# Performance work log

Measured on AMD Instinct MI355X. Metric: run time of the kernel, lower is better.

## Reference

```python
import jax, jax.numpy as jnp
import numpy as np

MAX_H = 512
MAX_W = 512
N_INST = 100
MASK_HW = 28


def _bilinear_sample(img, gx, gy):
    """grid_sample, mode='bilinear', padding_mode='zeros', align_corners=False.
    img: [B, H, W] float; gx, gy: [B, Ho, Wo] normalized coords in [-1, 1].
    Returns [B, Ho, Wo].
    """
    H, W = img.shape[1], img.shape[2]
    # unnormalize (align_corners=False)
    x = (gx + 1.0) * (W * 0.5) - 0.5
    y = (gy + 1.0) * (H * 0.5) - 0.5
    x0f = jnp.floor(x)
    y0f = jnp.floor(y)
    x0 = x0f.astype(jnp.int32)
    y0 = y0f.astype(jnp.int32)
    x1 = x0 + 1
    y1 = y0 + 1
    wx1 = x - x0f
    wx0 = 1.0 - wx1
    wy1 = y - y0f
    wy0 = 1.0 - wy1

    def gather(yi, xi):
        valid = (yi >= 0) & (yi < H) & (xi >= 0) & (xi < W)
        yc = jnp.clip(yi, 0, H - 1)
        xc = jnp.clip(xi, 0, W - 1)
        v = jax.vmap(lambda im, yy, xx: im[yy, xx])(img, yc, xc)
        return jnp.where(valid, v, jnp.zeros((), img.dtype))

    v00 = gather(y0, x0)
    v01 = gather(y0, x1)
    v10 = gather(y1, x0)
    v11 = gather(y1, x1)
    return (v00 * (wy0 * wx0) + v01 * (wy0 * wx1)
            + v10 * (wy1 * wx0) + v11 * (wy1 * wx1))


def setup_inputs() -> dict:
    key = jax.random.key(0)
    k1, k2, k3 = jax.random.split(key, 3)
    masks = jax.random.uniform(k1, (N_INST, 1, MASK_HW, MASK_HW), dtype=jnp.float32)
    # valid boxes inside the 512x512 canvas: x1 > x0, y1 > y0
    cxy = jax.random.uniform(k2, (N_INST, 2), minval=80.0, maxval=432.0)
    wh = jax.random.uniform(k3, (N_INST, 2), minval=32.0, maxval=256.0)
    x0y0 = jnp.clip(cxy - wh * 0.5, 0.0, MAX_W - 1.0)
    x1y1 = jnp.clip(cxy + wh * 0.5, 1.0, MAX_W - 1.0)
    boxes = jnp.concatenate([x0y0, x1y1], axis=1).astype(jnp.float32)
    return {"masks": masks, "boxes": boxes}


def reference(masks, boxes) -> jnp.ndarray:
    N, C, H, W = masks.shape
    m = masks.reshape(N * C, H, W).astype(jnp.float32)
    b = boxes.reshape(-1, 4)
    x0 = b[:, 0:1]
    y0 = b[:, 1:2]
    x1 = b[:, 2:3] + 1e-5
    y1 = b[:, 3:4] + 1e-5
    img_y = jnp.arange(MAX_H, dtype=jnp.float32) + 0.5  # [MAX_H]
    img_x = jnp.arange(MAX_W, dtype=jnp.float32) + 0.5  # [MAX_W]
    gy1d = (img_y[None, :] - y0) / (y1 - y0) * 2.0 - 1.0  # [B, MAX_H]
    gx1d = (img_x[None, :] - x0) / (x1 - x0) * 2.0 - 1.0  # [B, MAX_W]
    B = N * C
    gx = jnp.broadcast_to(gx1d[:, None, :], (B, MAX_H, MAX_W))
    gy = jnp.broadcast_to(gy1d[:, :, None], (B, MAX_H, MAX_W))
    out = _bilinear_sample(m, gx, gy)  # [B, MAX_H, MAX_W]
    return out.reshape(N, C, MAX_H, MAX_W)
```

## Files before the change

### kernel.cpp

```cpp
#include <hip/hip_runtime.h>

#define MASK_HW 28
#define OUT_H 512
#define OUT_W 512
#define ROWS_PER_BLOCK 16

__global__ __launch_bounds__(256) void paste_masks_kernel(
    const float* __restrict__ masks,
    const float* __restrict__ boxes,
    float* __restrict__ out)
{
    __shared__ float sm[31][33];
    const int n   = blockIdx.y;
    const int tid = threadIdx.x;

    for (int i = tid; i < 31 * 33; i += 256) ((float*)sm)[i] = 0.0f;
    __syncthreads();
    const float* mptr = masks + (size_t)n * (MASK_HW * MASK_HW);
    for (int i = tid; i < MASK_HW * MASK_HW; i += 256) {
        int r = i / MASK_HW;
        int c = i - r * MASK_HW;
        sm[r + 1][c + 1] = mptr[i];
    }

    const float bx0 = boxes[4 * n + 0];
    const float by0 = boxes[4 * n + 1];
    const float bx1 = boxes[4 * n + 2] + 1e-5f;
    const float by1 = boxes[4 * n + 3] + 1e-5f;
    const float sxf = 28.0f / (bx1 - bx0);
    const float syf = 28.0f / (by1 - by0);
    __syncthreads();

    const int row0 = blockIdx.x * ROWS_PER_BLOCK;
    float* outn = out + (size_t)n * (OUT_H * OUT_W);

    const int chunks = ROWS_PER_BLOCK * (OUT_W / 4);
    for (int cid = tid; cid < chunks; cid += 256) {
        const int r   = cid >> 7;
        const int xq  = cid & 127;
        const int row = row0 + r;

        const float ys = ((float)row + 0.5f - by0) * syf - 0.5f;
        float4 v = make_float4(0.f, 0.f, 0.f, 0.f);

        if (ys > -1.0f && ys < 28.0f) {
            const float y0f = floorf(ys);
            const int   y0i = (int)y0f;
            const float wy1 = ys - y0f;
            const float wy0 = 1.0f - wy1;
            const float* r0 = &sm[y0i + 1][0];
            const float* r1 = &sm[y0i + 2][0];

            const float xbase = (float)(xq * 4) + 0.5f - bx0;
            float res[4];
            #pragma unroll
            for (int j = 0; j < 4; ++j) {
                const float xs = (xbase + (float)j) * sxf - 0.5f;
                float val = 0.0f;
                if (xs > -1.0f && xs < 28.0f) {
                    const float x0f = floorf(xs);
                    const int   x0i = (int)x0f;
                    const float wx1 = xs - x0f;
                    const float wx0 = 1.0f - wx1;
                    const float v00 = r0[x0i + 1];
                    const float v01 = r0[x0i + 2];
                    const float v10 = r1[x0i + 1];
                    const float v11 = r1[x0i + 2];
                    val = wy0 * (wx0 * v00 + wx1 * v01) +
                          wy1 * (wx0 * v10 + wx1 * v11);
                }
                res[j] = val;
            }
            v = make_float4(res[0], res[1], res[2], res[3]);
        }
        *reinterpret_cast<float4*>(outn + (size_t)row * OUT_W + xq * 4) = v;
    }
}

extern "C" void kernel_launch(void* const* d_in, const int* in_sizes, int n_in,
                              void* d_out, int out_size, void* d_ws, size_t ws_size,
                              hipStream_t stream) {
    const float* masks = (const float*)d_in[0];
    const float* boxes = (const float*)d_in[1];
    float* out = (float*)d_out;

    dim3 grid(OUT_H / ROWS_PER_BLOCK, 100);
    dim3 block(256);
    paste_masks_kernel<<<grid, block, 0, stream>>>(masks, boxes, out);
}
```

Measured before the change: 112.5 us.

## Split into bulk zero-fill kernel and box-restricted bilinear paste kernel

The single kernel that interpolated every output pixel is replaced by two launches. A grid-stride kernel writes zeros over the whole output with float4 stores, then a second kernel computes bilinear values only inside each box's clipped row and column range. Row tiles that fall outside the box exit early, and shared-memory loading moves after that bounds check. The cost is a second launch, pixels inside each box being written twice, and scalar rather than float4 stores in the paste kernel.

Measured after the change: 121.9 us. +8.3%, slower.

```diff
diff --git a/kernel.cpp b/kernel.cpp
--- a/kernel.cpp
+++ b/kernel.cpp
@@ -3,25 +3,24 @@
 #define MASK_HW 28
 #define OUT_H 512
 #define OUT_W 512
-#define ROWS_PER_BLOCK 16
+#define N_INST 100
+#define ROWS_PER_TILE 16
 
-__global__ __launch_bounds__(256) void paste_masks_kernel(
+__global__ __launch_bounds__(256) void zero_fill_kernel(float4* __restrict__ out, int n4)
+{
+    const int stride = gridDim.x * 256;
+    const float4 z = make_float4(0.f, 0.f, 0.f, 0.f);
+    for (int i = blockIdx.x * 256 + threadIdx.x; i < n4; i += stride)
+        out[i] = z;
+}
+
+__global__ __launch_bounds__(256) void paste_box_kernel(
     const float* __restrict__ masks,
     const float* __restrict__ boxes,
     float* __restrict__ out)
 {
-    __shared__ float sm[31][33];
-    const int n   = blockIdx.y;
+    const int n   = blockIdx.x;
     const int tid = threadIdx.x;
-
-    for (int i = tid; i < 31 * 33; i += 256) ((float*)sm)[i] = 0.0f;
-    __syncthreads();
-    const float* mptr = masks + (size_t)n * (MASK_HW * MASK_HW);
-    for (int i = tid; i < MASK_HW * MASK_HW; i += 256) {
-        int r = i / MASK_HW;
-        int c = i - r * MASK_HW;
-        sm[r + 1][c + 1] = mptr[i];
-    }
 
     const float bx0 = boxes[4 * n + 0];
     const float by0 = boxes[4 * n + 1];
@@ -29,51 +28,60 @@
     const float by1 = boxes[4 * n + 3] + 1e-5f;
     const float sxf = 28.0f / (bx1 - bx0);
     const float syf = 28.0f / (by1 - by0);
+    const float inv_sx = (bx1 - bx0) * (1.0f / 28.0f);
+    const float inv_sy = (by1 - by0) * (1.0f / 28.0f);
+
+    const float xlo = bx0 - 0.5f - 0.5f * inv_sx;
+    const float xhi = bx0 - 0.5f + 28.5f * inv_sx;
+    const float ylo = by0 - 0.5f - 0.5f * inv_sy;
+    const float yhi = by0 - 0.5f + 28.5f * inv_sy;
+
+    const int clo = max(0, (int)floorf(xlo));
+    const int chi = min(OUT_W, (int)ceilf(xhi) + 1);
+    const int rlo = max(0, (int)floorf(ylo));
+    const int rhi = min(OUT_H, (int)ceilf(yhi) + 1);
+
+    const int r0 = rlo + blockIdx.y * ROWS_PER_TILE;
+    if (r0 >= rhi) return;
+    const int r1 = min(r0 + ROWS_PER_TILE, rhi);
+
+    __shared__ float sm[MASK_HW + 2][MASK_HW + 5];
+    for (int i = tid; i < (MASK_HW + 2) * (MASK_HW + 5); i += 256)
+        ((float*)sm)[i] = 0.0f;
+    __syncthreads();
+    const float* mptr = masks + (size_t)n * (MASK_HW * MASK_HW);
+    for (int i = tid; i < MASK_HW * MASK_HW; i += 256) {
+        const int r = i / MASK_HW;
+        const int c = i - r * MASK_HW;
+        sm[r + 1][c + 1] = mptr[i];
+    }
     __syncthreads();
 
-    const int row0 = blockIdx.x * ROWS_PER_BLOCK;
     float* outn = out + (size_t)n * (OUT_H * OUT_W);
 
-    const int chunks = ROWS_PER_BLOCK * (OUT_W / 4);
-    for (int cid = tid; cid < chunks; cid += 256) {
-        const int r   = cid >> 7;
-        const int xq  = cid & 127;
-        const int row = row0 + r;
+    for (int row = r0; row < r1; ++row) {
+        const float ys = ((float)row + 0.5f - by0) * syf - 0.5f;
+        if (ys <= -1.0f || ys >= 28.0f) continue;
+        const float y0f = floorf(ys);
+        const int   y0i = (int)y0f;
+        const float wy1 = ys - y0f;
+        const float wy0 = 1.0f - wy1;
+        const float* rA = &sm[y0i + 1][0];
+        const float* rB = &sm[y0i + 2][0];
 
-        const float ys = ((float)row + 0.5f - by0) * syf - 0.5f;
-        float4 v = make_float4(0.f, 0.f, 0.f, 0.f);
-
-        if (ys > -1.0f && ys < 28.0f) {
-            const float y0f = floorf(ys);
-            const int   y0i = (int)y0f;
-            const float wy1 = ys - y0f;
-            const float wy0 = 1.0f - wy1;
-            const float* r0 = &sm[y0i + 1][0];
-            const float* r1 = &sm[y0i + 2][0];
-
-            const float xbase = (float)(xq * 4) + 0.5f - bx0;
-            float res[4];
-            #pragma unroll
-            for (int j = 0; j < 4; ++j) {
-                const float xs = (xbase + (float)j) * sxf - 0.5f;
-                float val = 0.0f;
-                if (xs > -1.0f && xs < 28.0f) {
-                    const float x0f = floorf(xs);
-                    const int   x0i = (int)x0f;
-                    const float wx1 = xs - x0f;
-                    const float wx0 = 1.0f - wx1;
-                    const float v00 = r0[x0i + 1];
-                    const float v01 = r0[x0i + 2];
-                    const float v10 = r1[x0i + 1];
-                    const float v11 = r1[x0i + 2];
-                    val = wy0 * (wx0 * v00 + wx1 * v01) +
-                          wy1 * (wx0 * v10 + wx1 * v11);
-                }
-                res[j] = val;
+        for (int c = clo + tid; c < chi; c += 256) {
+            const float xs = ((float)c + 0.5f - bx0) * sxf - 0.5f;
+            float val = 0.0f;
+            if (xs > -1.0f && xs < 28.0f) {
+                const float x0f = floorf(xs);
+                const int   x0i = (int)x0f;
+                const float wx1 = xs - x0f;
+                const float wx0 = 1.0f - wx1;
+                val = wy0 * (wx0 * rA[x0i + 1] + wx1 * rA[x0i + 2]) +
+                      wy1 * (wx0 * rB[x0i + 1] + wx1 * rB[x0i + 2]);
             }
-            v = make_float4(res[0], res[1], res[2], res[3]);
+            outn[(size_t)row * OUT_W + c] = val;
         }
-        *reinterpret_cast<float4*>(outn + (size_t)row * OUT_W + xq * 4) = v;
     }
 }
 
@@ -84,7 +92,8 @@
     const float* boxes = (const float*)d_in[1];
     float* out = (float*)d_out;
 
-    dim3 grid(OUT_H / ROWS_PER_BLOCK, 100);
-    dim3 block(256);
-    paste_masks_kernel<<<grid, block, 0, stream>>>(masks, boxes, out);
+    const int n4 = N_INST * OUT_H * OUT_W / 4;
+    zero_fill_kernel<<<dim3(2048), dim3(256), 0, stream>>>((float4*)out, n4);
+
+    paste_box_kernel<<<dim3(N_INST, 17), dim3(256), 0, stream>>>(masks, boxes, out);
 }
```

## Drop shared-memory staging and gather mask texels directly from global

Applied to the files above, without the earlier changes.

Removes the per-block shared-memory tile, its zero-fill and both barriers. Each thread now reads the four mask texels straight from global memory (served by cache), using clamped indices with zeroed weights for border handling. The grid becomes one float4 per thread with a flat 1D launch, and threads whose row falls outside the box store zeros and exit early. The cost is more global and cache loads per output in exchange for less block setup and synchronisation in a store-bound kernel.

Measured after the change: 117.9 us. +4.8%, slower.

```diff
diff --git a/kernel.cpp b/kernel.cpp
--- a/kernel.cpp
+++ b/kernel.cpp
@@ -3,78 +3,70 @@
 #define MASK_HW 28
 #define OUT_H 512
 #define OUT_W 512
-#define ROWS_PER_BLOCK 16
+#define N_INST 100
 
-__global__ __launch_bounds__(256) void paste_masks_kernel(
+typedef __attribute__((ext_vector_type(4))) float f32x4;
+
+__global__ __launch_bounds__(256) void fused_paste_kernel(
     const float* __restrict__ masks,
     const float* __restrict__ boxes,
-    float* __restrict__ out)
+    f32x4* __restrict__ out)
 {
-    __shared__ float sm[31][33];
-    const int n   = blockIdx.y;
-    const int tid = threadIdx.x;
+    const int bid = blockIdx.x;
+    const int n   = bid >> 8;
+    const int idx = ((bid & 255) << 8) | threadIdx.x;
+    const int row = idx >> 7;
+    const int xq  = idx & 127;
 
-    for (int i = tid; i < 31 * 33; i += 256) ((float*)sm)[i] = 0.0f;
-    __syncthreads();
-    const float* mptr = masks + (size_t)n * (MASK_HW * MASK_HW);
-    for (int i = tid; i < MASK_HW * MASK_HW; i += 256) {
-        int r = i / MASK_HW;
-        int c = i - r * MASK_HW;
-        sm[r + 1][c + 1] = mptr[i];
+    f32x4* outp = out + ((size_t)n << 16) + idx;
+
+    const float by0 = boxes[4 * n + 1];
+    const float by1 = boxes[4 * n + 3] + 1e-5f;
+    const float syf = 28.0f / (by1 - by0);
+    const float ys  = ((float)row + 0.5f - by0) * syf - 0.5f;
+
+    if (ys <= -1.0f || ys >= 28.0f) {
+        *outp = (f32x4)0.0f;
+        return;
     }
 
     const float bx0 = boxes[4 * n + 0];
-    const float by0 = boxes[4 * n + 1];
     const float bx1 = boxes[4 * n + 2] + 1e-5f;
-    const float by1 = boxes[4 * n + 3] + 1e-5f;
     const float sxf = 28.0f / (bx1 - bx0);
-    const float syf = 28.0f / (by1 - by0);
-    __syncthreads();
 
-    const int row0 = blockIdx.x * ROWS_PER_BLOCK;
-    float* outn = out + (size_t)n * (OUT_H * OUT_W);
+    const float y0f = floorf(ys);
+    const int   y0i = (int)y0f;
+    const float wy1 = ys - y0f;
+    const float wy0 = 1.0f - wy1;
+    const float wyA = (y0i >= 0)  ? wy0 : 0.0f;
+    const float wyB = (y0i <= 26) ? wy1 : 0.0f;
+    const int   yA  = max(y0i, 0);
+    const int   yB  = min(y0i + 1, MASK_HW - 1);
+    const float* mrowA = masks + (size_t)n * (MASK_HW * MASK_HW) + yA * MASK_HW;
+    const float* mrowB = masks + (size_t)n * (MASK_HW * MASK_HW) + yB * MASK_HW;
 
-    const int chunks = ROWS_PER_BLOCK * (OUT_W / 4);
-    for (int cid = tid; cid < chunks; cid += 256) {
-        const int r   = cid >> 7;
-        const int xq  = cid & 127;
-        const int row = row0 + r;
-
-        const float ys = ((float)row + 0.5f - by0) * syf - 0.5f;
-        float4 v = make_float4(0.f, 0.f, 0.f, 0.f);
-
-        if (ys > -1.0f && ys < 28.0f) {
-            const float y0f = floorf(ys);
-            const int   y0i = (int)y0f;
-            const float wy1 = ys - y0f;
-            const float wy0 = 1.0f - wy1;
-            const float* r0 = &sm[y0i + 1][0];
-            const float* r1 = &sm[y0i + 2][0];
-
-            const float xbase = (float)(xq * 4) + 0.5f - bx0;
-            float res[4];
-            #pragma unroll
-            for (int j = 0; j < 4; ++j) {
-                const float xs = (xbase + (float)j) * sxf - 0.5f;
-                float val = 0.0f;
-                if (xs > -1.0f && xs < 28.0f) {
-                    const float x0f = floorf(xs);
-                    const int   x0i = (int)x0f;
-                    const float wx1 = xs - x0f;
-                    const float wx0 = 1.0f - wx1;
-                    const float v00 = r0[x0i + 1];
-                    const float v01 = r0[x0i + 2];
-                    const float v10 = r1[x0i + 1];
-                    const float v11 = r1[x0i + 2];
-                    val = wy0 * (wx0 * v00 + wx1 * v01) +
-                          wy1 * (wx0 * v10 + wx1 * v11);
-                }
-                res[j] = val;
-            }
-            v = make_float4(res[0], res[1], res[2], res[3]);
+    const float xbase = (float)(xq * 4) + 0.5f - bx0;
+    float res[4];
+    #pragma unroll
+    for (int j = 0; j < 4; ++j) {
+        const float xs = (xbase + (float)j) * sxf - 0.5f;
+        float v = 0.0f;
+        if (xs > -1.0f && xs < 28.0f) {
+            const float x0f = floorf(xs);
+            const int   x0i = (int)x0f;
+            const float wx1 = xs - x0f;
+            const float wx0 = 1.0f - wx1;
+            const float wxA = (x0i >= 0)  ? wx0 : 0.0f;
+            const float wxB = (x0i <= 26) ? wx1 : 0.0f;
+            const int   xA  = max(x0i, 0);
+            const int   xB  = min(x0i + 1, MASK_HW - 1);
+            v = wyA * (wxA * mrowA[xA] + wxB * mrowA[xB]) +
+                wyB * (wxA * mrowB[xA] + wxB * mrowB[xB]);
         }
-        *reinterpret_cast<float4*>(outn + (size_t)row * OUT_W + xq * 4) = v;
+        res[j] = v;
     }
+    f32x4 o; o.x = res[0]; o.y = res[1]; o.z = res[2]; o.w = res[3];
+    *outp = o;
 }
 
 extern "C" void kernel_launch(void* const* d_in, const int* in_sizes, int n_in,
@@ -82,9 +74,7 @@
                               hipStream_t stream) {
     const float* masks = (const float*)d_in[0];
     const float* boxes = (const float*)d_in[1];
-    float* out = (float*)d_out;
 
-    dim3 grid(OUT_H / ROWS_PER_BLOCK, 100);
-    dim3 block(256);
-    paste_masks_kernel<<<grid, block, 0, stream>>>(masks, boxes, out);
+    fused_paste_kernel<<<dim3(N_INST * 256), dim3(256), 0, stream>>>(
+        masks, boxes, (f32x4*)d_out);
 }
```
